# Kernel tuning notes

Measured on AMD Instinct MI355X. Metric: run time of the kernel, lower is better.

The kernel has to match this reference:

```python
import jax, jax.numpy as jnp
import numpy as np

EPS = 1e-12

def _natural_vvg_sym(x):
    """Natural vector visibility graph for one example.
    x: [S, D]. Returns symmetric 0/1 adjacency [S, S] = vg + vg.T (vg upper-triangular).
    Node a sees node b (a<b) iff for all a<c<b:
        y_c < y_b + (y_a - y_b) * (b - c) / (b - a),  y_k = <x_k, x_b> / ||x_b||
    """
    S = x.shape[0]
    t = jnp.arange(S, dtype=x.dtype)
    norms = jnp.maximum(jnp.linalg.norm(x, axis=-1), EPS)        # [S]
    Y = (x @ x.T) / norms[:, None]                                # Y[b,c] = <x_c,x_b>/||x_b||
    d = jnp.diagonal(Y)                                           # y_b = ||x_b||, [S]
    ta = t[:, None, None]   # a axis
    tb = t[None, :, None]   # b axis
    tc = t[None, None, :]   # c axis
    denom = jnp.where(tb != ta, tb - ta, jnp.ones((), x.dtype))   # avoid 0/0 on diagonal
    # visibility line at time c for pair (a,b): [S,S,S] indexed [a,b,c]
    line = d[None, :, None] + (Y.T[:, :, None] - d[None, :, None]) * (tb - tc) / denom
    between = (tc > ta) & (tc < tb)                               # strict interior points
    blocked = jnp.any((Y[None, :, :] >= line) & between, axis=-1) # [a,b]
    upper = t[None, :] > t[:, None]                               # b > a
    vg = (upper & ~blocked).astype(x.dtype)                       # upper-triangular adjacency
    return vg + vg.T


def setup_inputs() -> dict:
    key = jax.random.key(0)
    k1, k2 = jax.random.split(key)
    token_embs = jax.random.normal(k1, (8, 256, 768), dtype=jnp.float32)
    W = jax.random.normal(k2, (768, 4), dtype=jnp.float32)
    return {"token_embs": token_embs, "W": W}


def reference(token_embs, W):
    # vg_sym: [B, S, S]
    vg_sym = jax.vmap(_natural_vvg_sym)(token_embs)
    # torch: out[i] = multi_dot([vg, example, W])[0] == vg_sym[0] @ example @ W
    row0 = vg_sym[:, 0, :]                          # [B, S]
    h = jnp.einsum('bs,bsd->bd', row0, token_embs)  # [B, 768]
    logits = h @ W                                  # [B, n_class]
    return jax.nn.log_softmax(logits, axis=-1)
```

## Files before the change

### kernel.cpp

```cpp
#include <hip/hip_runtime.h>
#include <hip/hip_bf16.h>

constexpr int S  = 256;
constexpr int D  = 768;
constexpr int KQ = 4;
constexpr int KS = D / KQ;
constexpr int CH = 96;
constexpr int GROWS = KQ * S;

typedef _Float16 half8  __attribute__((ext_vector_type(8)));
typedef _Float16 half4v __attribute__((ext_vector_type(4)));
typedef float    f32x4  __attribute__((ext_vector_type(4)));

__device__ const int TI_MAP[10] = {0,1,1,2,2,2,3,3,3,3};
__device__ const int TJ_MAP[10] = {0,0,1,0,1,2,0,1,2,3};

__global__ __launch_bounds__(256) void gram_kernel(const float* __restrict__ X,
                                                   const float* __restrict__ Wm,
                                                   float* __restrict__ G,
                                                   float* __restrict__ Ppart) {
    const int ti    = TI_MAP[blockIdx.x];
    const int tj    = TJ_MAP[blockIdx.x];
    const int batch = blockIdx.y;
    const int kq    = blockIdx.z;
    const bool diag = (ti == tj);

    const float* Xq = X + (size_t)batch * S * D + kq * KS;

    __shared__ _Float16 AhS[64][104], AlS[64][104], BhS[64][104], BlS[64][104];
    __shared__ float Ws[192][4];

    const int t    = threadIdx.x;
    const int srow = t >> 2;
    const int sk   = (t & 3) * 24;

    if (diag && t < 192)
        *(float4*)&Ws[t][0] = *(const float4*)(Wm + (size_t)(kq * KS + t) * 4);

    const float* pa = Xq + (size_t)(ti * 64 + srow) * D + sk;
    const float* pb = Xq + (size_t)(tj * 64 + srow) * D + sk;

    float4 va[6], vb[6], xva[6];
#pragma unroll
    for (int c = 0; c < 6; ++c) va[c] = *(const float4*)(pa + c * 4);
    if (!diag) {
#pragma unroll
        for (int c = 0; c < 6; ++c) vb[c] = *(const float4*)(pb + c * 4);
    }

    const int lane = t & 63;
    const int w    = t >> 6;
    const int rb   = (w >> 1) * 32;
    const int cb   = (w & 1) * 32;
    const int frow = lane & 15;
    const int fko  = (lane >> 4) * 8;

    f32x4 acc00 = {}, acc01 = {}, acc10 = {}, acc11 = {};
    float4 pacc = make_float4(0.f, 0.f, 0.f, 0.f);

    for (int ch = 0; ch < 2; ++ch) {
        if (ch) __syncthreads();
#pragma unroll
        for (int c = 0; c < 6; ++c) {
            const int ko = sk + c * 4;
            const float4 a = va[c];
            half4v ha, la;
            ha.x = (_Float16)a.x; la.x = (_Float16)(a.x - (float)ha.x);
            ha.y = (_Float16)a.y; la.y = (_Float16)(a.y - (float)ha.y);
            ha.z = (_Float16)a.z; la.z = (_Float16)(a.z - (float)ha.z);
            ha.w = (_Float16)a.w; la.w = (_Float16)(a.w - (float)ha.w);
            *(half4v*)&AhS[srow][ko] = ha;
            *(half4v*)&AlS[srow][ko] = la;
        }
        if (!diag) {
#pragma unroll
            for (int c = 0; c < 6; ++c) {
                const int ko = sk + c * 4;
                const float4 bq = vb[c];
                half4v hb, lb;
                hb.x = (_Float16)bq.x; lb.x = (_Float16)(bq.x - (float)hb.x);
                hb.y = (_Float16)bq.y; lb.y = (_Float16)(bq.y - (float)hb.y);
                hb.z = (_Float16)bq.z; lb.z = (_Float16)(bq.z - (float)hb.z);
                hb.w = (_Float16)bq.w; lb.w = (_Float16)(bq.w - (float)hb.w);
                *(half4v*)&BhS[srow][ko] = hb;
                *(half4v*)&BlS[srow][ko] = lb;
            }
        } else {
#pragma unroll
            for (int c = 0; c < 6; ++c) xva[c] = va[c];
        }
        if (ch == 0) {
#pragma unroll
            for (int c = 0; c < 6; ++c) va[c] = *(const float4*)(pa + CH + c * 4);
            if (!diag) {
#pragma unroll
                for (int c = 0; c < 6; ++c) vb[c] = *(const float4*)(pb + CH + c * 4);
            }
        }
        __syncthreads();

        if (diag) {
#pragma unroll
            for (int c = 0; c < 6; ++c) {
                const float xf[4] = {xva[c].x, xva[c].y, xva[c].z, xva[c].w};
#pragma unroll
                for (int q = 0; q < 4; ++q) {
                    const float4 wq = *(const float4*)&Ws[ch * CH + sk + c * 4 + q][0];
                    pacc.x = fmaf(xf[q], wq.x, pacc.x);
                    pacc.y = fmaf(xf[q], wq.y, pacc.y);
                    pacc.z = fmaf(xf[q], wq.z, pacc.z);
                    pacc.w = fmaf(xf[q], wq.w, pacc.w);
                }
            }
        }

        _Float16 (*Bh)[104] = diag ? AhS : BhS;
        _Float16 (*Bl)[104] = diag ? AlS : BlS;
#pragma unroll
        for (int ks = 0; ks < 3; ++ks) {
            const int k0 = ks * 32 + fko;
            const half8 ah0 = *(const half8*)&AhS[rb + frow][k0];
            const half8 al0 = *(const half8*)&AlS[rb + frow][k0];
            const half8 ah1 = *(const half8*)&AhS[rb + 16 + frow][k0];
            const half8 al1 = *(const half8*)&AlS[rb + 16 + frow][k0];
            const half8 bh0 = *(const half8*)&Bh[cb + frow][k0];
            const half8 bl0 = *(const half8*)&Bl[cb + frow][k0];
            const half8 bh1 = *(const half8*)&Bh[cb + 16 + frow][k0];
            const half8 bl1 = *(const half8*)&Bl[cb + 16 + frow][k0];
            acc00 = __builtin_amdgcn_mfma_f32_16x16x32_f16(ah0, bh0, acc00, 0, 0, 0);
            acc00 = __builtin_amdgcn_mfma_f32_16x16x32_f16(ah0, bl0, acc00, 0, 0, 0);
            acc00 = __builtin_amdgcn_mfma_f32_16x16x32_f16(al0, bh0, acc00, 0, 0, 0);
            acc01 = __builtin_amdgcn_mfma_f32_16x16x32_f16(ah0, bh1, acc01, 0, 0, 0);
            acc01 = __builtin_amdgcn_mfma_f32_16x16x32_f16(ah0, bl1, acc01, 0, 0, 0);
            acc01 = __builtin_amdgcn_mfma_f32_16x16x32_f16(al0, bh1, acc01, 0, 0, 0);
            acc10 = __builtin_amdgcn_mfma_f32_16x16x32_f16(ah1, bh0, acc10, 0, 0, 0);
            acc10 = __builtin_amdgcn_mfma_f32_16x16x32_f16(ah1, bl0, acc10, 0, 0, 0);
            acc10 = __builtin_amdgcn_mfma_f32_16x16x32_f16(al1, bh0, acc10, 0, 0, 0);
            acc11 = __builtin_amdgcn_mfma_f32_16x16x32_f16(ah1, bh1, acc11, 0, 0, 0);
            acc11 = __builtin_amdgcn_mfma_f32_16x16x32_f16(ah1, bl1, acc11, 0, 0, 0);
            acc11 = __builtin_amdgcn_mfma_f32_16x16x32_f16(al1, bh1, acc11, 0, 0, 0);
        }
    }

    if (diag) {
#pragma unroll
        for (int off = 1; off <= 2; off <<= 1) {
            pacc.x += __shfl_xor(pacc.x, off);
            pacc.y += __shfl_xor(pacc.y, off);
            pacc.z += __shfl_xor(pacc.z, off);
            pacc.w += __shfl_xor(pacc.w, off);
        }
        if ((t & 3) == 0)
            *(float4*)(Ppart + (((size_t)batch * S + ti * 64 + srow) * KQ + kq) * 4) = pacc;
    }

    float* gout = G + ((size_t)(batch * S + ti * 64 + rb + (lane >> 4) * 4) * KQ + kq) * S
                    + tj * 64 + cb + frow;
#pragma unroll
    for (int r = 0; r < 4; ++r) {
        gout[(size_t)r * GROWS]                    = acc00[r];
        gout[(size_t)r * GROWS + 16]               = acc01[r];
        gout[(size_t)(16 + r) * GROWS]             = acc10[r];
        gout[(size_t)(16 + r) * GROWS + 16]        = acc11[r];
    }
}

__device__ __forceinline__ void vis_one(const float* __restrict__ G,
                                        float* __restrict__ wv,
                                        int batch, int b, int lane) {
    const float* rbp = G + (size_t)(batch * S + b) * GROWS + 4 * lane;
    float4 s0 = make_float4(0.f, 0.f, 0.f, 0.f), s1 = s0, s2 = s0, s3 = s0;
    if (4 * lane <= b) {
        s0 = *(const float4*)(rbp + (size_t)0 * S);
        s1 = *(const float4*)(rbp + (size_t)1 * S);
        s2 = *(const float4*)(rbp + (size_t)2 * S);
        s3 = *(const float4*)(rbp + (size_t)3 * S);
    }
    float4 gs;
    gs.x = (s0.x + s1.x) + (s2.x + s3.x);
    gs.y = (s0.y + s1.y) + (s2.y + s3.y);
    gs.z = (s0.z + s1.z) + (s2.z + s3.z);
    gs.w = (s0.w + s1.w) + (s2.w + s3.w);

    const int bq = b & 3;
    float sel = (bq == 0) ? gs.x : ((bq == 1) ? gs.y : ((bq == 2) ? gs.z : gs.w));
    const float gb = __shfl(sel, b >> 2);
    const float g0 = __shfl(gs.x, 0);
    const float denom = (b > 0) ? (float)b : 1.0f;

    bool blocked = false;
    {
        const int c0 = 4 * lane;
#define VTEST(Q, GV) { const int c = c0 + (Q); \
        const float line = gb + ((g0 - gb) * (float)(b - c)) / denom; \
        if (c >= 1 && c < b && (GV) >= line) blocked = true; }
        VTEST(0, gs.x) VTEST(1, gs.y) VTEST(2, gs.z) VTEST(3, gs.w)
#undef VTEST
    }
    const bool visflag = (b >= 1) && !__any(blocked);

    if (lane == 0) wv[batch * S + b] = visflag ? 1.0f : 0.0f;
}

__global__ __launch_bounds__(256) void vis_kernel(const float* __restrict__ G,
                                                  float* __restrict__ wv) {
    const int batch = blockIdx.y;
    const int wave  = threadIdx.x >> 6;
    const int lane  = threadIdx.x & 63;
    const int u     = blockIdx.x * 4 + wave;

    vis_one(G, wv, batch, u, lane);
    vis_one(G, wv, batch, 255 - u, lane);
}

__global__ __launch_bounds__(256) void head_kernel(const float* __restrict__ Ppart,
                                                   const float* __restrict__ wv,
                                                   float* __restrict__ out) {
    const int batch = blockIdx.x;
    const int t     = threadIdx.x;
    const int wave  = t >> 6;
    const int lane  = t & 63;

    float4 acc = make_float4(0.f, 0.f, 0.f, 0.f);
    if (wv[batch * S + t] != 0.0f) {
        const float* pp = Ppart + ((size_t)batch * S + t) * (KQ * 4);
#pragma unroll
        for (int kq = 0; kq < KQ; ++kq) {
            const float4 p = *(const float4*)(pp + kq * 4);
            acc.x += p.x; acc.y += p.y; acc.z += p.z; acc.w += p.w;
        }
    }
#pragma unroll
    for (int off = 32; off; off >>= 1) {
        acc.x += __shfl_xor(acc.x, off);
        acc.y += __shfl_xor(acc.y, off);
        acc.z += __shfl_xor(acc.z, off);
        acc.w += __shfl_xor(acc.w, off);
    }

    __shared__ float4 lsh[4];
    if (lane == 0) lsh[wave] = acc;
    __syncthreads();

    if (t == 0) {
        const float l0 = ((lsh[0].x + lsh[1].x) + (lsh[2].x + lsh[3].x));
        const float l1 = ((lsh[0].y + lsh[1].y) + (lsh[2].y + lsh[3].y));
        const float l2 = ((lsh[0].z + lsh[1].z) + (lsh[2].z + lsh[3].z));
        const float l3 = ((lsh[0].w + lsh[1].w) + (lsh[2].w + lsh[3].w));
        const float m = fmaxf(fmaxf(l0, l1), fmaxf(l2, l3));
        const float lse = logf(expf(l0 - m) + expf(l1 - m) + expf(l2 - m) + expf(l3 - m));
        out[batch * 4 + 0] = l0 - m - lse;
        out[batch * 4 + 1] = l1 - m - lse;
        out[batch * 4 + 2] = l2 - m - lse;
        out[batch * 4 + 3] = l3 - m - lse;
    }
}

extern "C" void kernel_launch(void* const* d_in, const int* in_sizes, int n_in,
                              void* d_out, int out_size, void* d_ws, size_t ws_size,
                              hipStream_t stream) {
    const float* X  = (const float*)d_in[0];
    const float* Wm = (const float*)d_in[1];
    float* out = (float*)d_out;

    float* ws = (float*)d_ws;
    float* Ppart = ws;
    float* wv    = ws + 32768;
    float* G     = ws + 34816;

    gram_kernel<<<dim3(10, 8, 4), 256, 0, stream>>>(X, Wm, G, Ppart);
    vis_kernel <<<dim3(32, 8),    256, 0, stream>>>(G, wv);
    head_kernel<<<8,              256, 0, stream>>>(Ppart, wv, out);
}
```

Baseline: 18.22 us.

## Fuse visibility and head kernels into one per-batch block using shared memory

Merges the visibility test and the logits/log-softmax head into a single 1024-thread kernel with one block per batch, keeping the visibility flags in shared memory instead of global memory. This removes one kernel launch and the global round trip for the flags. In exchange the visibility work, previously spread over 256 blocks, now runs on only 8 blocks of 16 waves each, which process 16 rows serially and leave most of the GPU idle.

```diff
diff --git a/kernel.cpp b/kernel.cpp
--- a/kernel.cpp
+++ b/kernel.cpp
@@ -166,7 +166,7 @@
 }
 
 __device__ __forceinline__ void vis_one(const float* __restrict__ G,
-                                        float* __restrict__ wv,
+                                        float* __restrict__ wv_sh,
                                         int batch, int b, int lane) {
     const float* rbp = G + (size_t)(batch * S + b) * GROWS + 4 * lane;
     float4 s0 = make_float4(0.f, 0.f, 0.f, 0.f), s1 = s0, s2 = s0, s3 = s0;
@@ -199,47 +199,45 @@
     }
     const bool visflag = (b >= 1) && !__any(blocked);
 
-    if (lane == 0) wv[batch * S + b] = visflag ? 1.0f : 0.0f;
-}
-
-__global__ __launch_bounds__(256) void vis_kernel(const float* __restrict__ G,
-                                                  float* __restrict__ wv) {
-    const int batch = blockIdx.y;
-    const int wave  = threadIdx.x >> 6;
-    const int lane  = threadIdx.x & 63;
-    const int u     = blockIdx.x * 4 + wave;
-
-    vis_one(G, wv, batch, u, lane);
-    vis_one(G, wv, batch, 255 - u, lane);
-}
-
-__global__ __launch_bounds__(256) void head_kernel(const float* __restrict__ Ppart,
-                                                   const float* __restrict__ wv,
-                                                   float* __restrict__ out) {
+    if (lane == 0) wv_sh[b] = visflag ? 1.0f : 0.0f;
+}
+
+__global__ __launch_bounds__(1024) void vishead_kernel(const float* __restrict__ G,
+                                                       const float* __restrict__ Ppart,
+                                                       float* __restrict__ out) {
     const int batch = blockIdx.x;
     const int t     = threadIdx.x;
     const int wave  = t >> 6;
     const int lane  = t & 63;
 
+    __shared__ float wv_sh[S];
+    __shared__ float4 lsh[4];
+
+#pragma unroll
+    for (int j = 0; j < 16; ++j)
+        vis_one(G, wv_sh, batch, wave + 16 * j, lane);
+
+    __syncthreads();
+
     float4 acc = make_float4(0.f, 0.f, 0.f, 0.f);
-    if (wv[batch * S + t] != 0.0f) {
-        const float* pp = Ppart + ((size_t)batch * S + t) * (KQ * 4);
-#pragma unroll
-        for (int kq = 0; kq < KQ; ++kq) {
-            const float4 p = *(const float4*)(pp + kq * 4);
-            acc.x += p.x; acc.y += p.y; acc.z += p.z; acc.w += p.w;
-        }
-    }
-#pragma unroll
-    for (int off = 32; off; off >>= 1) {
-        acc.x += __shfl_xor(acc.x, off);
-        acc.y += __shfl_xor(acc.y, off);
-        acc.z += __shfl_xor(acc.z, off);
-        acc.w += __shfl_xor(acc.w, off);
-    }
-
-    __shared__ float4 lsh[4];
-    if (lane == 0) lsh[wave] = acc;
+    if (t < S) {
+        if (wv_sh[t] != 0.0f) {
+            const float* pp = Ppart + ((size_t)batch * S + t) * (KQ * 4);
+#pragma unroll
+            for (int kq = 0; kq < KQ; ++kq) {
+                const float4 p = *(const float4*)(pp + kq * 4);
+                acc.x += p.x; acc.y += p.y; acc.z += p.z; acc.w += p.w;
+            }
+        }
+#pragma unroll
+        for (int off = 32; off; off >>= 1) {
+            acc.x += __shfl_xor(acc.x, off);
+            acc.y += __shfl_xor(acc.y, off);
+            acc.z += __shfl_xor(acc.z, off);
+            acc.w += __shfl_xor(acc.w, off);
+        }
+        if (lane == 0) lsh[wave] = acc;
+    }
     __syncthreads();
 
     if (t == 0) {
@@ -265,10 +263,8 @@
 
     float* ws = (float*)d_ws;
     float* Ppart = ws;
-    float* wv    = ws + 32768;
-    float* G     = ws + 34816;
-
-    gram_kernel<<<dim3(10, 8, 4), 256, 0, stream>>>(X, Wm, G, Ppart);
-    vis_kernel <<<dim3(32, 8),    256, 0, stream>>>(G, wv);
-    head_kernel<<<8,              256, 0, stream>>>(Ppart, wv, out);
-}
+    float* G     = ws + 32768;
+
+    gram_kernel   <<<dim3(10, 8, 4), 256,  0, stream>>>(X, Wm, G, Ppart);
+    vishead_kernel<<<8,              1024, 0, stream>>>(G, Ppart, out);
+}
```

Result: slower. 29.02 us (+59.2%).
